# Performance work log

Measured on AMD Instinct MI355X. Metric: run time of the kernel, lower is better.

The kernel has to match this reference:

```python
import math
import jax, jax.numpy as jnp
import numpy as np

EMBED_DIM = 512
NUM_HEADS = 8
EDGE_VOC = 16
EDGE_PAD = 0
L, B = 512, 16


def setup_inputs() -> dict:
    key = jax.random.key(0)
    ks = jax.random.split(key, 8)
    x = jax.random.normal(ks[0], (L, B, EMBED_DIM), dtype=jnp.float32)
    edge = jax.random.randint(ks[1], (B, L, L), 0, EDGE_VOC, dtype=jnp.int32)
    key_padding_mask = jnp.zeros((B, L), dtype=bool)
    # causal additive mask, as from nn.Transformer.generate_square_subsequent_mask
    attn_mask = jnp.where(jnp.triu(jnp.ones((L, L), bool), k=1), -jnp.inf, 0.0).astype(jnp.float32)
    s = 1.0 / math.sqrt(EMBED_DIM)
    in_proj_w = jax.random.uniform(ks[2], (3 * EMBED_DIM, EMBED_DIM), jnp.float32, -s, s)
    in_proj_b = jnp.zeros((3 * EMBED_DIM,), jnp.float32)
    out_proj_w = jax.random.uniform(ks[3], (EMBED_DIM, EMBED_DIM), jnp.float32, -s, s)
    out_proj_b = jnp.zeros((EMBED_DIM,), jnp.float32)
    edge_emb = jax.random.normal(ks[4], (EDGE_VOC, NUM_HEADS), dtype=jnp.float32)
    edge_emb = edge_emb.at[EDGE_PAD].set(0.0)  # padding_idx row zeroed
    return {"x": x, "edge": edge, "key_padding_mask": key_padding_mask,
            "attn_mask": attn_mask, "in_proj_w": in_proj_w, "in_proj_b": in_proj_b,
            "out_proj_w": out_proj_w, "out_proj_b": out_proj_b, "edge_emb": edge_emb}


def reference(x, edge, key_padding_mask, attn_mask,
              in_proj_w, in_proj_b, out_proj_w, out_proj_b, edge_emb):
    length, bsz, embed_dim = x.shape
    H = edge_emb.shape[1]
    hd = embed_dim // H
    qkv = x @ in_proj_w.T + in_proj_b                       # (L, B, 3E)
    q, k, v = jnp.split(qkv, 3, axis=-1)
    # (L, B*H, hd) -> (B*H, L, hd)
    q = q.reshape(length, bsz * H, hd).transpose(1, 0, 2)
    k = k.reshape(length, bsz * H, hd).transpose(1, 0, 2)
    v = v.reshape(length, bsz * H, hd).transpose(1, 0, 2)
    # combine attn_mask with key padding
    mask = attn_mask[None]                                   # (1, L, L)
    kpm = jnp.broadcast_to(key_padding_mask[:, None, None, :],
                           (bsz, H, 1, length)).reshape(bsz * H, 1, length)
    mask = jnp.where(kpm, -jnp.inf, mask)                    # (B*H, 1/L, L)
    # edge bias: (B, L, L, H) -> (B*H, L, L)
    ebias = edge_emb[edge].transpose(0, 3, 1, 2).reshape(bsz * H, length, length)
    q = q / math.sqrt(hd)
    scores = jnp.einsum('bqd,bkd->bqk', q, k) + mask + ebias
    attn = jax.nn.softmax(scores, axis=-1)
    out = jnp.einsum('bqk,bkd->bqd', attn, v)                # (B*H, L, hd)
    out = out.transpose(1, 0, 2).reshape(length, bsz, embed_dim)
    return out @ out_proj_w.T + out_proj_b
```

## Files before the change

kernel.cpp:

```cpp
#include <hip/hip_runtime.h>
#include <hip/hip_bf16.h>


typedef __attribute__((ext_vector_type(8))) short bf16x8;
typedef __attribute__((ext_vector_type(4))) float f32x4;
typedef __attribute__((ext_vector_type(4))) int i32x4;

#define LOG2E 1.44269504088896340736f

__device__ inline void gll16(const void* g, const void* l) {
  __builtin_amdgcn_global_load_lds(
      (const __attribute__((address_space(1))) unsigned int*)g,
      (__attribute__((address_space(3))) unsigned int*)l, 16, 0, 0);
}

__device__ inline short f2bf(float x) {
  __hip_bfloat16 t = __float2bfloat16(x);
  return *reinterpret_cast<short*>(&t);
}

__device__ inline void cstore(__hip_bfloat16* C, size_t idx, float v) {
  C[idx] = __float2bfloat16(v);
}
__device__ inline void cstore(float* C, size_t idx, float v) { C[idx] = v; }

__global__ void cvt_pack(const float* __restrict__ x,
                         const float* __restrict__ w1,
                         const float* __restrict__ w2,
                         const int* __restrict__ edge,
                         __hip_bfloat16* __restrict__ xb,
                         __hip_bfloat16* __restrict__ w1b,
                         __hip_bfloat16* __restrict__ w2b,
                         unsigned int* __restrict__ epk) {
  const int blk = blockIdx.x;
  if (blk >= 2560) {
    const int t = (blk - 2560) * 256 + threadIdx.x;
    const int base = t * 8;
    const i32x4 a = *(const i32x4*)(edge + base);
    const i32x4 b = *(const i32x4*)(edge + base + 4);
    unsigned int w = 0;
#pragma unroll
    for (int j = 0; j < 4; j++) {
      w |= ((unsigned int)(a[j] & 15)) << (4 * j);
      w |= ((unsigned int)(b[j] & 15)) << (16 + 4 * j);
    }
    epk[t] = w;
    return;
  }
  const float* src;
  __hip_bfloat16* dst;
  int off;
  if (blk < 2048)      { src = x;  dst = xb;  off = blk; }
  else if (blk < 2432) { src = w1; dst = w1b; off = blk - 2048; }
  else                 { src = w2; dst = w2b; off = blk - 2432; }
  const int i = (off * 256 + threadIdx.x) * 8;
  const float4 a = *(const float4*)(src + i);
  const float4 b = *(const float4*)(src + i + 4);
  bf16x8 r;
  r[0] = f2bf(a.x); r[1] = f2bf(a.y); r[2] = f2bf(a.z); r[3] = f2bf(a.w);
  r[4] = f2bf(b.x); r[5] = f2bf(b.y); r[6] = f2bf(b.z); r[7] = f2bf(b.w);
  *(bf16x8*)(dst + i) = r;
}

template <int MT, int RB, typename TC>
__global__ __launch_bounds__(256, RB) void gemm_bt(
    const __hip_bfloat16* __restrict__ A,
    const __hip_bfloat16* __restrict__ W,
    const float* __restrict__ bias,
    TC* __restrict__ C, int N, int K) {
  constexpr int MI = MT / 32;
  __shared__ short As[MT * 32];
  __shared__ short Ws[128 * 32];
  const int tid = threadIdx.x;
  const int wave = tid >> 6, lane = tid & 63;
  const int c = lane & 15, quad = lane >> 4;
  const int nb = N >> 7;
  const int bx = blockIdx.x % nb, by = blockIdx.x / nb;
  const int m0 = by * MT, n0 = bx << 7;
  const int wm = wave >> 1, wn = wave & 1;

  f32x4 acc[MI][4] = {};
  const int ar = lane >> 2;
  const int ak = (lane & 3) * 8;

  for (int k0 = 0; k0 < K; k0 += 32) {
    __syncthreads();
#pragma unroll
    for (int i = 0; i < MT / 64; i++) {
      const int r0 = i * 64 + wave * 16;
      gll16(A + (size_t)(m0 + r0 + ar) * K + k0 + ak, &As[r0 * 32]);
    }
#pragma unroll
    for (int i = 0; i < 2; i++) {
      const int r0 = i * 64 + wave * 16;
      gll16(W + (size_t)(n0 + r0 + ar) * K + k0 + ak, &Ws[r0 * 32]);
    }
    __syncthreads();
    bf16x8 af[MI], bfr[4];
#pragma unroll
    for (int i = 0; i < MI; i++)
      af[i] = *(const bf16x8*)&As[(wm * (MT / 2) + i * 16 + c) * 32 + quad * 8];
#pragma unroll
    for (int j = 0; j < 4; j++)
      bfr[j] = *(const bf16x8*)&Ws[(wn * 64 + j * 16 + c) * 32 + quad * 8];
#pragma unroll
    for (int i = 0; i < MI; i++)
#pragma unroll
      for (int j = 0; j < 4; j++)
        acc[i][j] = __builtin_amdgcn_mfma_f32_16x16x32_bf16(af[i], bfr[j],
                                                            acc[i][j], 0, 0, 0);
  }
#pragma unroll
  for (int j = 0; j < 4; j++) {
    const int col = n0 + wn * 64 + j * 16 + c;
    const float bv = bias[col];
#pragma unroll
    for (int i = 0; i < MI; i++) {
      const int row = m0 + wm * (MT / 2) + i * 16 + quad * 4;
#pragma unroll
      for (int r = 0; r < 4; r++)
        cstore(C, (size_t)(row + r) * N + col, acc[i][j][r] + bv);
    }
  }
}

__global__ __launch_bounds__(256, 4) void attn_kernel(
    const __hip_bfloat16* __restrict__ qkv,
    const unsigned short* __restrict__ ep16,
    const float* __restrict__ edge_emb,
    __hip_bfloat16* __restrict__ attn_out) {
  __shared__ short Ks[64 * 72];
  __shared__ short Vt[64 * 72];
  __shared__ short Ps[4][16 * 72];
  __shared__ float eeS[16];

  const int tid = threadIdx.x;
  const int wave = tid >> 6, lane = tid & 63;
  const int c = lane & 15, quad = lane >> 4;
  const int i = blockIdx.x;
  constexpr int pi[8] = {0, 7, 1, 6, 2, 5, 3, 4};
  const int qb = pi[((i & 7) + (i >> 8)) & 7];
  const int bh = i >> 3;
  const int b = bh >> 3, h = bh & 7;
  const int colq = h * 64;

  if (tid < 16) eeS[tid] = (edge_emb[tid * 8 + h] - 16.0f) * LOG2E;

  const int q_g = (qb << 6) + wave * 16 + c;
  bf16x8 qf0, qf1;
  {
    const __hip_bfloat16* qp_ = qkv + (size_t)(q_g * 16 + b) * 1536 + colq;
    qf0 = *(const bf16x8*)(qp_ + quad * 8);
    qf1 = *(const bf16x8*)(qp_ + 32 + quad * 8);
  }
  float lsum = 0.f;
  f32x4 o[4] = {};
  const int enib = (b * 512 + q_g) * 512;

  const int r2 = tid >> 3;
  const int cc = (tid & 7) * 8;
  const int kcol0 = ((r2 << 1) & 7) | (((r2 >> 2) ^ (cc >> 3)) << 3);
  const size_t sbase0 = (size_t)((r2 * 2) * 16 + b) * 1536 + colq + cc;
  bf16x8 kreg[2], vreg[2];
  kreg[0] = *(const bf16x8*)(qkv + sbase0 + 512);
  vreg[0] = *(const bf16x8*)(qkv + sbase0 + 1024);
  kreg[1] = *(const bf16x8*)(qkv + sbase0 + 24576 + 512);
  vreg[1] = *(const bf16x8*)(qkv + sbase0 + 24576 + 1024);

  __syncthreads();

  const int nkt = qb + 1;
  for (int kt = 0; kt < nkt; kt++) {
    const int k0 = kt << 6;
    if (kt) __syncthreads();
    *(bf16x8*)&Ks[(r2 * 2) * 72 + cc] = kreg[0];
    *(bf16x8*)&Ks[(r2 * 2 + 1) * 72 + cc] = kreg[1];
#pragma unroll
    for (int j = 0; j < 8; j++) {
      short2 p;
      p.x = vreg[0][j];
      p.y = vreg[1][j];
      *(short2*)&Vt[(cc + j) * 72 + kcol0] = p;
    }
    if (kt + 1 < nkt) {
      const size_t nb_ = sbase0 + (size_t)(kt + 1) * 64 * 24576;
      kreg[0] = *(const bf16x8*)(qkv + nb_ + 512);
      vreg[0] = *(const bf16x8*)(qkv + nb_ + 1024);
      kreg[1] = *(const bf16x8*)(qkv + nb_ + 24576 + 512);
      vreg[1] = *(const bf16x8*)(qkv + nb_ + 24576 + 1024);
    }
    unsigned int ew[4];
#pragma unroll
    for (int mt = 0; mt < 4; mt++)
      ew[mt] = ep16[(enib + k0 + mt * 16 + quad * 4) >> 2];
    __syncthreads();

    f32x4 st[4];
#pragma unroll
    for (int mt = 0; mt < 4; mt++) {
      const bf16x8 ka = *(const bf16x8*)&Ks[(mt * 16 + c) * 72 + quad * 8];
      const bf16x8 kb = *(const bf16x8*)&Ks[(mt * 16 + c) * 72 + 32 + quad * 8];
      f32x4 z = {0.f, 0.f, 0.f, 0.f};
      z = __builtin_amdgcn_mfma_f32_16x16x32_bf16(ka, qf0, z, 0, 0, 0);
      st[mt] = __builtin_amdgcn_mfma_f32_16x16x32_bf16(kb, qf1, z, 0, 0, 0);
    }
    float rsum = 0.0f;
#pragma unroll
    for (int mt = 0; mt < 4; mt++) {
      short4 pk;
#pragma unroll
      for (int r = 0; r < 4; r++) {
        const int key = k0 + mt * 16 + quad * 4 + r;
        const int code = (ew[mt] >> (4 * r)) & 15;
        const float p = (key <= q_g)
            ? exp2f(fmaf(st[mt][r], 0.125f * LOG2E, eeS[code]))
            : 0.0f;
        rsum += p;
        ((short*)&pk)[r] = f2bf(p);
      }
      *(short4*)&Ps[wave][c * 72 + mt * 16 + quad * 4] = pk;
    }
    lsum += rsum;
    const bf16x8 pa0 = *(const bf16x8*)&Ps[wave][c * 72 + quad * 8];
    const bf16x8 pa1 = *(const bf16x8*)&Ps[wave][c * 72 + 32 + quad * 8];
#pragma unroll
    for (int nt = 0; nt < 4; nt++) {
      const int n = nt * 16 + c;
      const bf16x8 vb0 = *(const bf16x8*)&Vt[n * 72 + ((quad ^ (n >> 3)) << 3)];
      const bf16x8 vb1 =
          *(const bf16x8*)&Vt[n * 72 + (((4 + quad) ^ (n >> 3)) << 3)];
      o[nt] = __builtin_amdgcn_mfma_f32_16x16x32_bf16(pa0, vb0, o[nt], 0, 0, 0);
      o[nt] = __builtin_amdgcn_mfma_f32_16x16x32_bf16(pa1, vb1, o[nt], 0, 0, 0);
    }
  }

  float l = lsum;
  l += __shfl_xor(l, 16);
  l += __shfl_xor(l, 32);
  float lr[4];
#pragma unroll
  for (int r = 0; r < 4; r++) lr[r] = __shfl(l, quad * 4 + r, 16);
  const int qrow0 = (qb << 6) + wave * 16 + quad * 4;
#pragma unroll
  for (int nt = 0; nt < 4; nt++)
#pragma unroll
    for (int r = 0; r < 4; r++)
      attn_out[(size_t)((qrow0 + r) * 16 + b) * 512 + colq + nt * 16 + c] =
          __float2bfloat16(o[nt][r] / lr[r]);
}

extern "C" void kernel_launch(void* const* d_in, const int* in_sizes, int n_in,
                              void* d_out, int out_size, void* d_ws, size_t ws_size,
                              hipStream_t stream) {
  const float* x    = (const float*)d_in[0];
  const int* edge   = (const int*)d_in[1];
  const float* ipw  = (const float*)d_in[4];
  const float* ipb  = (const float*)d_in[5];
  const float* opw  = (const float*)d_in[6];
  const float* opb  = (const float*)d_in[7];
  const float* eemb = (const float*)d_in[8];
  float* out = (float*)d_out;

  __hip_bfloat16* qkv  = (__hip_bfloat16*)d_ws;
  __hip_bfloat16* attn = qkv + (size_t)8192 * 1536;
  __hip_bfloat16* xb   = attn + (size_t)8192 * 512;
  __hip_bfloat16* w1b  = xb + (size_t)8192 * 512;
  __hip_bfloat16* w2b  = w1b + (size_t)1536 * 512;
  unsigned int* epk    = (unsigned int*)(w2b + (size_t)512 * 512);

  cvt_pack<<<4608, 256, 0, stream>>>(x, ipw, opw, edge, xb, w1b, w2b, epk);
  gemm_bt<128, 3, __hip_bfloat16>
      <<<768, 256, 0, stream>>>(xb, w1b, ipb, qkv, 1536, 512);
  attn_kernel<<<1024, 256, 0, stream>>>(qkv, (const unsigned short*)epk, eemb,
                                        attn);
  gemm_bt<64, 2, float>
      <<<512, 256, 0, stream>>>(attn, w2b, opb, out, 512, 512);
}
```

Baseline: 155.9 us.

## Read raw int32 edge codes directly in attention and drop the nibble-packing pass

Removes the separate pass that packed the int32 edge tensor into 4-bit nibbles. The attention kernel now loads the int32 edge codes directly as 16-byte vectors. It also remaps block indices so each XCD handles whole batches, aiming for better L2 locality on K/V. This avoids a full read of the edge tensor plus a packed write and read, but the attention kernel now reads about 8x more edge bytes (only the causal half) from HBM.

```diff
diff --git a/kernel.cpp b/kernel.cpp
--- a/kernel.cpp
+++ b/kernel.cpp
@@ -24,29 +24,11 @@
 }
 __device__ inline void cstore(float* C, size_t idx, float v) { C[idx] = v; }
 
-__global__ void cvt_pack(const float* __restrict__ x,
-                         const float* __restrict__ w1,
-                         const float* __restrict__ w2,
-                         const int* __restrict__ edge,
-                         __hip_bfloat16* __restrict__ xb,
-                         __hip_bfloat16* __restrict__ w1b,
-                         __hip_bfloat16* __restrict__ w2b,
-                         unsigned int* __restrict__ epk) {
+__global__ void cvt3(const float* __restrict__ x, const float* __restrict__ w1,
+                     const float* __restrict__ w2, __hip_bfloat16* __restrict__ xb,
+                     __hip_bfloat16* __restrict__ w1b,
+                     __hip_bfloat16* __restrict__ w2b) {
   const int blk = blockIdx.x;
-  if (blk >= 2560) {
-    const int t = (blk - 2560) * 256 + threadIdx.x;
-    const int base = t * 8;
-    const i32x4 a = *(const i32x4*)(edge + base);
-    const i32x4 b = *(const i32x4*)(edge + base + 4);
-    unsigned int w = 0;
-#pragma unroll
-    for (int j = 0; j < 4; j++) {
-      w |= ((unsigned int)(a[j] & 15)) << (4 * j);
-      w |= ((unsigned int)(b[j] & 15)) << (16 + 4 * j);
-    }
-    epk[t] = w;
-    return;
-  }
   const float* src;
   __hip_bfloat16* dst;
   int off;
@@ -126,7 +108,7 @@
 
 __global__ __launch_bounds__(256, 4) void attn_kernel(
     const __hip_bfloat16* __restrict__ qkv,
-    const unsigned short* __restrict__ ep16,
+    const int* __restrict__ edge,
     const float* __restrict__ edge_emb,
     __hip_bfloat16* __restrict__ attn_out) {
   __shared__ short Ks[64 * 72];
@@ -139,9 +121,11 @@
   const int c = lane & 15, quad = lane >> 4;
   const int i = blockIdx.x;
   constexpr int pi[8] = {0, 7, 1, 6, 2, 5, 3, 4};
-  const int qb = pi[((i & 7) + (i >> 8)) & 7];
-  const int bh = i >> 3;
-  const int b = bh >> 3, h = bh & 7;
+  const int xcd = i & 7;
+  const int j = i >> 3;
+  const int qb = pi[j & 7];
+  const int h = (j >> 3) & 7;
+  const int b = xcd + ((j >> 6) << 3);
   const int colq = h * 64;
 
   if (tid < 16) eeS[tid] = (edge_emb[tid * 8 + h] - 16.0f) * LOG2E;
@@ -155,7 +139,7 @@
   }
   float lsum = 0.f;
   f32x4 o[4] = {};
-  const int enib = (b * 512 + q_g) * 512;
+  const int* erow = edge + ((size_t)(b * 512 + q_g)) * 512;
 
   const int r2 = tid >> 3;
   const int cc = (tid & 7) * 8;
@@ -176,11 +160,11 @@
     *(bf16x8*)&Ks[(r2 * 2) * 72 + cc] = kreg[0];
     *(bf16x8*)&Ks[(r2 * 2 + 1) * 72 + cc] = kreg[1];
 #pragma unroll
-    for (int j = 0; j < 8; j++) {
+    for (int j2 = 0; j2 < 8; j2++) {
       short2 p;
-      p.x = vreg[0][j];
-      p.y = vreg[1][j];
-      *(short2*)&Vt[(cc + j) * 72 + kcol0] = p;
+      p.x = vreg[0][j2];
+      p.y = vreg[1][j2];
+      *(short2*)&Vt[(cc + j2) * 72 + kcol0] = p;
     }
     if (kt + 1 < nkt) {
       const size_t nb_ = sbase0 + (size_t)(kt + 1) * 64 * 24576;
@@ -189,10 +173,10 @@
       kreg[1] = *(const bf16x8*)(qkv + nb_ + 24576 + 512);
       vreg[1] = *(const bf16x8*)(qkv + nb_ + 24576 + 1024);
     }
-    unsigned int ew[4];
+    i32x4 e4[4];
 #pragma unroll
     for (int mt = 0; mt < 4; mt++)
-      ew[mt] = ep16[(enib + k0 + mt * 16 + quad * 4) >> 2];
+      e4[mt] = *(const i32x4*)(erow + k0 + mt * 16 + quad * 4);
     __syncthreads();
 
     f32x4 st[4];
@@ -211,9 +195,8 @@
 #pragma unroll
       for (int r = 0; r < 4; r++) {
         const int key = k0 + mt * 16 + quad * 4 + r;
-        const int code = (ew[mt] >> (4 * r)) & 15;
         const float p = (key <= q_g)
-            ? exp2f(fmaf(st[mt][r], 0.125f * LOG2E, eeS[code]))
+            ? exp2f(fmaf(st[mt][r], 0.125f * LOG2E, eeS[e4[mt][r] & 15]))
             : 0.0f;
         rsum += p;
         ((short*)&pk)[r] = f2bf(p);
@@ -266,13 +249,11 @@
   __hip_bfloat16* xb   = attn + (size_t)8192 * 512;
   __hip_bfloat16* w1b  = xb + (size_t)8192 * 512;
   __hip_bfloat16* w2b  = w1b + (size_t)1536 * 512;
-  unsigned int* epk    = (unsigned int*)(w2b + (size_t)512 * 512);
-
-  cvt_pack<<<4608, 256, 0, stream>>>(x, ipw, opw, edge, xb, w1b, w2b, epk);
+
+  cvt3<<<2560, 256, 0, stream>>>(x, ipw, opw, xb, w1b, w2b);
   gemm_bt<128, 3, __hip_bfloat16>
       <<<768, 256, 0, stream>>>(xb, w1b, ipb, qkv, 1536, 512);
-  attn_kernel<<<1024, 256, 0, stream>>>(qkv, (const unsigned short*)epk, eemb,
-                                        attn);
+  attn_kernel<<<1024, 256, 0, stream>>>(qkv, edge, eemb, attn);
   gemm_bt<64, 2, float>
       <<<512, 256, 0, stream>>>(attn, w2b, opb, out, 512, 512);
 }
```

After: 153.5 us. About the same (-1.5%).
